# Kernel tuning notes

Hardware: AMD Instinct MI355X
Metric: run time of the kernel (lower is better)

Reference implementation:

```python
import jax, jax.numpy as jnp
import numpy as np

GAMMA = 1.0 / 512.0  # RBF bandwidth, 1/d_feat


def _rbf_kernel(X, Z, gamma):
    # X: [N, d], Z: [M, d] -> K: [N, M], K[i,j] = exp(-gamma * ||x_i - z_j||^2)
    xn = jnp.sum(X * X, axis=1, keepdims=True)        # [N, 1]
    zn = jnp.sum(Z * Z, axis=1, keepdims=True).T      # [1, M]
    sq = xn + zn - 2.0 * (X @ Z.T)                    # [N, M]
    return jnp.exp(-gamma * jnp.maximum(sq, 0.0))


def setup_inputs() -> dict:
    key = jax.random.key(0)
    k1, k2, k3, k4, k5 = jax.random.split(key, 5)
    N, d, M = 8192, 512, 4096
    inputs = jax.random.normal(k1, (M, d), dtype=jnp.float32)
    X = jax.random.normal(k2, (N, d), dtype=jnp.float32)
    # SVM labels in {-1, +1}
    Y = jnp.where(jax.random.uniform(k3, (N, 1)) > 0.5, 1.0, -1.0).astype(jnp.float32)
    a = jax.random.normal(k4, (N, 1), dtype=jnp.float32) * 0.1
    b = jax.random.normal(k5, (1, 1), dtype=jnp.float32)
    return {"inputs": inputs, "X": X, "Y": Y, "a": a, "b": b}


def reference(inputs, X, Y, a, b):
    # K: [N, M]; weighted sum over support vectors N, then add bias, transpose.
    K = _rbf_kernel(X, inputs, GAMMA)                 # [N, M]
    s = jnp.sum(a * Y * K, axis=0)                    # [M]
    out = (s + b)                                     # [1, M] via broadcast with [1,1]
    return out.T                                      # [M, 1]
```

## Files before the change

kernel.cpp:

```cpp
#include <hip/hip_runtime.h>
#include <hip/hip_bf16.h>
#include <stdint.h>

#define GAMMA_F 0.001953125f

static constexpr int N_SV = 8192;
static constexpr int M_Q  = 4096;
static constexpr int DIM  = 512;

typedef __bf16 bf16x8 __attribute__((ext_vector_type(8)));
typedef float  f32x4  __attribute__((ext_vector_type(4)));

#define GLB const __attribute__((address_space(1))) void
#define LDS __attribute__((address_space(3))) void

__global__ __launch_bounds__(64) void svm_prep(
    const float* __restrict__ Z, const float* __restrict__ X,
    const float* __restrict__ Y, const float* __restrict__ a,
    __bf16* __restrict__ Xb, __bf16* __restrict__ Zb,
    float* __restrict__ xn, float* __restrict__ zn, float* __restrict__ w)
{
    const int r = blockIdx.x;
    const int t = threadIdx.x;
    const float* src;
    __bf16* dst;
    if (r < N_SV) { src = X + (size_t)r * DIM; dst = Xb + (size_t)r * DIM; }
    else          { src = Z + (size_t)(r - N_SV) * DIM; dst = Zb + (size_t)(r - N_SV) * DIM; }

    float4 v0 = ((const float4*)src)[t * 2];
    float4 v1 = ((const float4*)src)[t * 2 + 1];

    float s = v0.x*v0.x + v0.y*v0.y + v0.z*v0.z + v0.w*v0.w
            + v1.x*v1.x + v1.y*v1.y + v1.z*v1.z + v1.w*v1.w;

    __bf16 h[8];
    h[0] = (__bf16)v0.x; h[1] = (__bf16)v0.y; h[2] = (__bf16)v0.z; h[3] = (__bf16)v0.w;
    h[4] = (__bf16)v1.x; h[5] = (__bf16)v1.y; h[6] = (__bf16)v1.z; h[7] = (__bf16)v1.w;
    uint4 bits;
    __builtin_memcpy(&bits, h, 16);
    ((uint4*)dst)[t] = bits;

    #pragma unroll
    for (int o = 32; o > 0; o >>= 1) s += __shfl_xor(s, o);

    if (t == 0) {
        if (r < N_SV) { xn[r] = s; w[r] = a[r] * Y[r]; }
        else          { zn[r - N_SV] = s; }
    }
}

__global__ __launch_bounds__(256) void svm_init(float* __restrict__ out,
                                                const float* __restrict__ b)
{
    int j = blockIdx.x * 256 + threadIdx.x;
    if (j < M_Q) out[j] = b[0];
}

__global__ __launch_bounds__(256) void svm_main(
    const __bf16* __restrict__ Xb, const __bf16* __restrict__ Zb,
    const float* __restrict__ xn, const float* __restrict__ zn,
    const float* __restrict__ w, float* __restrict__ out)
{
    __shared__ __bf16 As[128 * 32];
    __shared__ __bf16 Bs[128 * 32];

    const int tid  = threadIdx.x;
    const int lane = tid & 63;
    const int wid  = tid >> 6;
    const int wr   = wid >> 1;
    const int wc   = wid & 1;

    const int bi = blockIdx.y;
    const int bj = blockIdx.x;
    const int iBase = bi * 128;
    const int jBase = bj * 128;

    f32x4 acc[4][4];
    #pragma unroll
    for (int m = 0; m < 4; ++m)
        #pragma unroll
        for (int n = 0; n < 4; ++n)
            acc[m][n] = (f32x4)(0.0f);

    const int srow = tid >> 2;
    const int scb  = (tid & 3) * 16;
    const int sce  = scb >> 1;

    const int lrow = lane & 15;
    const int lk   = (lane >> 4) * 8;

    for (int k0 = 0; k0 < DIM; k0 += 32) {
        #pragma unroll
        for (int q = 0; q < 2; ++q) {
            const int row = q * 64 + srow;
            const __bf16* sa = Xb + (size_t)(iBase + row) * DIM + k0 + sce;
            __builtin_amdgcn_global_load_lds((GLB*)sa,
                (LDS*)((char*)As + q * 4096 + tid * 16), 16, 0, 0);
            const __bf16* sb = Zb + (size_t)(jBase + row) * DIM + k0 + sce;
            __builtin_amdgcn_global_load_lds((GLB*)sb,
                (LDS*)((char*)Bs + q * 4096 + tid * 16), 16, 0, 0);
        }
        __syncthreads();

        bf16x8 af[4], bfr[4];
        #pragma unroll
        for (int m = 0; m < 4; ++m)
            af[m] = *(const bf16x8*)(As + (wr * 64 + m * 16 + lrow) * 32 + lk);
        #pragma unroll
        for (int n = 0; n < 4; ++n)
            bfr[n] = *(const bf16x8*)(Bs + (wc * 64 + n * 16 + lrow) * 32 + lk);

        #pragma unroll
        for (int m = 0; m < 4; ++m)
            #pragma unroll
            for (int n = 0; n < 4; ++n)
                acc[m][n] = __builtin_amdgcn_mfma_f32_16x16x32_bf16(
                    af[m], bfr[n], acc[m][n], 0, 0, 0);

        __syncthreads();
    }

    const int rg   = lane >> 4;
    const int lcol = lane & 15;

    float wv[16], xv[16];
    #pragma unroll
    for (int m = 0; m < 4; ++m)
        #pragma unroll
        for (int r = 0; r < 4; ++r) {
            const int i = iBase + wr * 64 + m * 16 + rg * 4 + r;
            wv[m * 4 + r] = w[i];
            xv[m * 4 + r] = xn[i];
        }

    #pragma unroll
    for (int n = 0; n < 4; ++n) {
        const int j = jBase + wc * 64 + n * 16 + lcol;
        const float znj = zn[j];
        float cs = 0.0f;
        #pragma unroll
        for (int m = 0; m < 4; ++m)
            #pragma unroll
            for (int r = 0; r < 4; ++r) {
                float d = xv[m * 4 + r] + znj - 2.0f * acc[m][n][r];
                d = fmaxf(d, 0.0f);
                cs += wv[m * 4 + r] * __expf(-GAMMA_F * d);
            }
        cs += __shfl_xor(cs, 16);
        cs += __shfl_xor(cs, 32);
        if (lane < 16) atomicAdd(out + j, cs);
    }
}

extern "C" void kernel_launch(void* const* d_in, const int* in_sizes, int n_in,
                              void* d_out, int out_size, void* d_ws, size_t ws_size,
                              hipStream_t stream)
{
    const float* Z = (const float*)d_in[0];
    const float* X = (const float*)d_in[1];
    const float* Y = (const float*)d_in[2];
    const float* a = (const float*)d_in[3];
    const float* b = (const float*)d_in[4];
    float* out = (float*)d_out;

    char* ws = (char*)d_ws;
    __bf16* Xb = (__bf16*)ws;
    __bf16* Zb = (__bf16*)(ws + 8ull * 1024 * 1024);
    float*  xn = (float*)(ws + 12ull * 1024 * 1024);
    float*  zn = xn + N_SV;
    float*  w  = zn + M_Q;

    svm_prep<<<N_SV + M_Q, 64, 0, stream>>>(Z, X, Y, a, Xb, Zb, xn, zn, w);
    svm_init<<<(M_Q + 255) / 256, 256, 0, stream>>>(out, b);
    svm_main<<<dim3(M_Q / 128, N_SV / 128), 256, 0, stream>>>(Xb, Zb, xn, zn, w, out);
}
```

Measured before the change: 133.1 us.

## Double-buffer LDS tiles with XOR swizzle, fuse init into prep, use exp2

The main GEMM loop now double-buffers the LDS tiles so the next K-slice's global-to-LDS loads are issued before the current slice is computed. It also applies an XOR swizzle to the LDS layout to reduce bank conflicts on fragment reads. The output-init kernel is folded into the prep kernel, which now handles four rows per block with coalesced loads and stores. The exponential is rewritten as exp2 with a prescaled constant. Together these aim to hide load latency and cut launch overhead, at the cost of doubling LDS use, which may reduce occupancy.

```diff
diff --git a/kernel.cpp b/kernel.cpp
--- a/kernel.cpp
+++ b/kernel.cpp
@@ -3,6 +3,7 @@
 #include <stdint.h>
 
 #define GAMMA_F 0.001953125f
+#define C2EXP (-0.0028179443441958f)
 
 static constexpr int N_SV = 8192;
 static constexpr int M_Q  = 4096;
@@ -14,46 +15,43 @@
 #define GLB const __attribute__((address_space(1))) void
 #define LDS __attribute__((address_space(3))) void
 
-__global__ __launch_bounds__(64) void svm_prep(
+__global__ __launch_bounds__(256) void svm_prep(
     const float* __restrict__ Z, const float* __restrict__ X,
     const float* __restrict__ Y, const float* __restrict__ a,
+    const float* __restrict__ b,
     __bf16* __restrict__ Xb, __bf16* __restrict__ Zb,
-    float* __restrict__ xn, float* __restrict__ zn, float* __restrict__ w)
+    float* __restrict__ xn, float* __restrict__ zn, float* __restrict__ w,
+    float* __restrict__ out)
 {
-    const int r = blockIdx.x;
-    const int t = threadIdx.x;
+    const int r = blockIdx.x * 4 + (threadIdx.x >> 6);
+    const int t = threadIdx.x & 63;
     const float* src;
     __bf16* dst;
     if (r < N_SV) { src = X + (size_t)r * DIM; dst = Xb + (size_t)r * DIM; }
     else          { src = Z + (size_t)(r - N_SV) * DIM; dst = Zb + (size_t)(r - N_SV) * DIM; }
 
-    float4 v0 = ((const float4*)src)[t * 2];
-    float4 v1 = ((const float4*)src)[t * 2 + 1];
+    const float4* row4 = (const float4*)src;
+    float4 v0 = row4[t];
+    float4 v1 = row4[t + 64];
 
     float s = v0.x*v0.x + v0.y*v0.y + v0.z*v0.z + v0.w*v0.w
             + v1.x*v1.x + v1.y*v1.y + v1.z*v1.z + v1.w*v1.w;
 
-    __bf16 h[8];
-    h[0] = (__bf16)v0.x; h[1] = (__bf16)v0.y; h[2] = (__bf16)v0.z; h[3] = (__bf16)v0.w;
-    h[4] = (__bf16)v1.x; h[5] = (__bf16)v1.y; h[6] = (__bf16)v1.z; h[7] = (__bf16)v1.w;
-    uint4 bits;
-    __builtin_memcpy(&bits, h, 16);
-    ((uint4*)dst)[t] = bits;
+    __bf16 h0[4] = {(__bf16)v0.x, (__bf16)v0.y, (__bf16)v0.z, (__bf16)v0.w};
+    __bf16 h1[4] = {(__bf16)v1.x, (__bf16)v1.y, (__bf16)v1.z, (__bf16)v1.w};
+    uint2 b0, b1;
+    __builtin_memcpy(&b0, h0, 8);
+    __builtin_memcpy(&b1, h1, 8);
+    ((uint2*)dst)[t]      = b0;
+    ((uint2*)dst)[t + 64] = b1;
 
     #pragma unroll
     for (int o = 32; o > 0; o >>= 1) s += __shfl_xor(s, o);
 
     if (t == 0) {
         if (r < N_SV) { xn[r] = s; w[r] = a[r] * Y[r]; }
-        else          { zn[r - N_SV] = s; }
+        else          { int m = r - N_SV; zn[m] = s; out[m] = b[0]; }
     }
-}
-
-__global__ __launch_bounds__(256) void svm_init(float* __restrict__ out,
-                                                const float* __restrict__ b)
-{
-    int j = blockIdx.x * 256 + threadIdx.x;
-    if (j < M_Q) out[j] = b[0];
 }
 
 __global__ __launch_bounds__(256) void svm_main(
@@ -61,8 +59,8 @@
     const float* __restrict__ xn, const float* __restrict__ zn,
     const float* __restrict__ w, float* __restrict__ out)
 {
-    __shared__ __bf16 As[128 * 32];
-    __shared__ __bf16 Bs[128 * 32];
+    __shared__ __bf16 As[2 * 128 * 32];
+    __shared__ __bf16 Bs[2 * 128 * 32];
 
     const int tid  = threadIdx.x;
     const int lane = tid & 63;
@@ -70,10 +68,8 @@
     const int wr   = wid >> 1;
     const int wc   = wid & 1;
 
-    const int bi = blockIdx.y;
-    const int bj = blockIdx.x;
-    const int iBase = bi * 128;
-    const int jBase = bj * 128;
+    const int iBase = blockIdx.y * 128;
+    const int jBase = blockIdx.x * 128;
 
     f32x4 acc[4][4];
     #pragma unroll
@@ -82,33 +78,44 @@
         for (int n = 0; n < 4; ++n)
             acc[m][n] = (f32x4)(0.0f);
 
-    const int srow = tid >> 2;
-    const int scb  = (tid & 3) * 16;
-    const int sce  = scb >> 1;
+    const int srow   = tid >> 2;
+    const int schunk = (tid & 3) ^ ((tid >> 3) & 3);
+    const int sce    = schunk * 8;
 
     const int lrow = lane & 15;
-    const int lk   = (lane >> 4) * 8;
+    const int rsw  = (lrow >> 1) & 3;
+    const int lkb  = ((lane >> 4) ^ rsw) * 16;
 
-    for (int k0 = 0; k0 < DIM; k0 += 32) {
+    auto stage = [&](int buf, int k0) {
         #pragma unroll
         for (int q = 0; q < 2; ++q) {
             const int row = q * 64 + srow;
             const __bf16* sa = Xb + (size_t)(iBase + row) * DIM + k0 + sce;
             __builtin_amdgcn_global_load_lds((GLB*)sa,
-                (LDS*)((char*)As + q * 4096 + tid * 16), 16, 0, 0);
+                (LDS*)((char*)As + buf * 8192 + q * 4096 + tid * 16), 16, 0, 0);
             const __bf16* sb = Zb + (size_t)(jBase + row) * DIM + k0 + sce;
             __builtin_amdgcn_global_load_lds((GLB*)sb,
-                (LDS*)((char*)Bs + q * 4096 + tid * 16), 16, 0, 0);
+                (LDS*)((char*)Bs + buf * 8192 + q * 4096 + tid * 16), 16, 0, 0);
         }
-        __syncthreads();
+    };
+
+    stage(0, 0);
+    __syncthreads();
+
+    #pragma unroll
+    for (int kt = 0; kt < 16; ++kt) {
+        const int buf = kt & 1;
+        if (kt < 15) stage(buf ^ 1, (kt + 1) * 32);
 
         bf16x8 af[4], bfr[4];
         #pragma unroll
         for (int m = 0; m < 4; ++m)
-            af[m] = *(const bf16x8*)(As + (wr * 64 + m * 16 + lrow) * 32 + lk);
+            af[m] = *(const bf16x8*)((const char*)As + buf * 8192
+                        + (wr * 64 + m * 16 + lrow) * 64 + lkb);
         #pragma unroll
         for (int n = 0; n < 4; ++n)
-            bfr[n] = *(const bf16x8*)(Bs + (wc * 64 + n * 16 + lrow) * 32 + lk);
+            bfr[n] = *(const bf16x8*)((const char*)Bs + buf * 8192
+                        + (wc * 64 + n * 16 + lrow) * 64 + lkb);
 
         #pragma unroll
         for (int m = 0; m < 4; ++m)
@@ -144,7 +151,7 @@
             for (int r = 0; r < 4; ++r) {
                 float d = xv[m * 4 + r] + znj - 2.0f * acc[m][n][r];
                 d = fmaxf(d, 0.0f);
-                cs += wv[m * 4 + r] * __expf(-GAMMA_F * d);
+                cs += wv[m * 4 + r] * exp2f(C2EXP * d);
             }
         cs += __shfl_xor(cs, 16);
         cs += __shfl_xor(cs, 32);
@@ -170,7 +177,6 @@
     float*  zn = xn + N_SV;
     float*  w  = zn + M_Q;
 
-    svm_prep<<<N_SV + M_Q, 64, 0, stream>>>(Z, X, Y, a, Xb, Zb, xn, zn, w);
-    svm_init<<<(M_Q + 255) / 256, 256, 0, stream>>>(out, b);
+    svm_prep<<<(N_SV + M_Q) / 4, 256, 0, stream>>>(Z, X, Y, a, b, Xb, Zb, xn, zn, w, out);
     svm_main<<<dim3(M_Q / 128, N_SV / 128), 256, 0, stream>>>(Xb, Zb, xn, zn, w, out);
 }
```

Result: slower. 136.8 us (+2.8%).
